# Kernel tuning notes

Measured on AMD Instinct MI355X. Metric: run time of the kernel, lower is better.

The kernel has to match this reference:

```python
import jax, jax.numpy as jnp
import numpy as np

B = 32768          # batch (replay-buffer minibatch)
OBS, ACT = 17, 6   # HalfCheetah-style dims
IN = OBS + ACT
H = 256            # hidden width hard-coded in the module
N = 10             # num_q_nets


def setup_inputs() -> dict:
    key = jax.random.key(0)
    ks = jax.random.split(key, 8)
    # PyTorch Linear default init: U(-1/sqrt(fan_in), 1/sqrt(fan_in)); scale randn similarly.
    s1, s2, s3 = 1.0 / np.sqrt(IN), 1.0 / np.sqrt(H), 1.0 / np.sqrt(H)
    return {
        "state": jax.random.normal(ks[0], (B, OBS), dtype=jnp.float32),
        "action": jax.random.uniform(ks[1], (B, ACT), dtype=jnp.float32, minval=-1.0, maxval=1.0),
        "W1": jax.random.normal(ks[2], (N, IN, H), dtype=jnp.float32) * s1,
        "b1": jax.random.normal(ks[3], (N, H), dtype=jnp.float32) * s1,
        "W2": jax.random.normal(ks[4], (N, H, H), dtype=jnp.float32) * s2,
        "b2": jax.random.normal(ks[5], (N, H), dtype=jnp.float32) * s2,
        "W3": jax.random.normal(ks[6], (N, H, 1), dtype=jnp.float32) * s3,
        "b3": jax.random.normal(ks[7], (N, 1), dtype=jnp.float32) * s3,
    }


def reference(state, action, W1, b1, W2, b2, W3, b3):
    # x: [B, OBS+ACT]
    x = jnp.concatenate([state, action], axis=1)
    # batched-over-ensemble GEMMs; n=ensemble member, b=batch
    h1 = jax.nn.relu(jnp.einsum("bi,nih->nbh", x, W1) + b1[:, None, :])   # [N,B,H]
    h2 = jax.nn.relu(jnp.einsum("nbh,nho->nbo", h1, W2) + b2[:, None, :])  # [N,B,H]
    out = jnp.einsum("nbh,nho->nbo", h2, W3) + b3[:, None, :]              # [N,B,1]
    return out
```

## Files before the change

### kernel.cpp

```cpp
#include <hip/hip_runtime.h>


typedef __attribute__((ext_vector_type(8))) short bf16x8;
typedef __attribute__((ext_vector_type(4))) float f32x4;

#define B_TOTAL 32768
#define NQ 10
#define HDIM 256
#define BT 128

__device__ __forceinline__ unsigned short f2bf(float f) {
  unsigned int u = __float_as_uint(f);
  u = u + 0x7FFFu + ((u >> 16) & 1u);
  return (unsigned short)(u >> 16);
}
__device__ __forceinline__ float bf2f(unsigned short h) {
  return __uint_as_float(((unsigned int)h) << 16);
}


__global__ void pack_x_kernel(const float* __restrict__ state,
                              const float* __restrict__ action,
                              unsigned short* __restrict__ xp) {
  int t = blockIdx.x * 256 + threadIdx.x;
  if (t >= B_TOTAL * 32) return;
  int b = t >> 5, k = t & 31;
  float v = 0.f;
  if (k < 17) v = state[b * 17 + k];
  else if (k < 23) v = action[b * 6 + (k - 17)];
  xp[t] = f2bf(v);
}

__global__ void pack_w1_kernel(const float* __restrict__ W1, unsigned short* __restrict__ w1p) {
  int t = blockIdx.x * 256 + threadIdx.x;
  if (t >= NQ * 16 * 64) return;
  int lane = t & 63;
  int ct = (t >> 6) & 15;
  int n = t >> 10;
  int c = ct * 16 + (lane & 15);
  int q = lane >> 4;
#pragma unroll
  for (int j = 0; j < 8; j++) {
    int k = q * 8 + j;
    float v = (k < 23) ? W1[(n * 23 + k) * 256 + c] : 0.f;
    w1p[(size_t)t * 8 + j] = f2bf(v);
  }
}

__global__ void pack_w2_kernel(const float* __restrict__ W2, unsigned short* __restrict__ w2p) {
  int t = blockIdx.x * 256 + threadIdx.x;
  if (t >= NQ * 8 * 16 * 64) return;
  int lane = t & 63;
  int ct = (t >> 6) & 15;
  int kt = (t >> 10) & 7;
  int n = t >> 13;
  int c = ct * 16 + (lane & 15);
  int q = lane >> 4;
#pragma unroll
  for (int j = 0; j < 8; j++) {
    int k = kt * 32 + q * 8 + j;
    w2p[(size_t)t * 8 + j] = f2bf(W2[((size_t)n * 256 + k) * 256 + c]);
  }
}

__global__ __launch_bounds__(256, 2) void fused_ensemble_kernel(
    const unsigned short* __restrict__ xp,
    const unsigned short* __restrict__ w1p,
    const float* __restrict__ b1,
    const unsigned short* __restrict__ w2p,
    const float* __restrict__ b2,
    const float* __restrict__ W3,
    const float* __restrict__ b3,
    float* __restrict__ out) {
  __shared__ __align__(16) unsigned short xs[BT * 40];
  __shared__ __align__(16) unsigned short h1s[BT * 264];
  __shared__ float w3s[HDIM];

  const int tid = threadIdx.x;
  const int lane = tid & 63;
  const int wave = tid >> 6;
  const int m = lane & 15;
  const int q = lane >> 4;

  const int n = blockIdx.x >> 8;
  const int tile = blockIdx.x & 255;
  const int row0 = tile * BT;

  {
    const uint4* src = (const uint4*)(xp + (size_t)row0 * 32);
#pragma unroll
    for (int i = 0; i < 2; i++) {
      int idx = tid + i * 256;
      int r = idx >> 2, c4 = idx & 3;
      uint4 v = src[idx];
      *(uint4*)&xs[r * 40 + c4 * 8] = v;
    }
  }
  if (tid < HDIM) w3s[tid] = W3[n * HDIM + tid];
  __syncthreads();

  f32x4 acc[8][4];
#pragma unroll
  for (int a = 0; a < 8; a++)
#pragma unroll
    for (int b = 0; b < 4; b++) acc[a][b] = (f32x4){0.f, 0.f, 0.f, 0.f};

  {
    bf16x8 bfrag[4];
#pragma unroll
    for (int cti = 0; cti < 4; cti++) {
      int ct = wave * 4 + cti;
      bfrag[cti] = *(const bf16x8*)(w1p + (((size_t)n * 16 + ct) * 64 + lane) * 8);
    }
#pragma unroll
    for (int mt = 0; mt < 8; mt++) {
      bf16x8 afrag = *(const bf16x8*)&xs[(mt * 16 + m) * 40 + q * 8];
#pragma unroll
      for (int cti = 0; cti < 4; cti++)
        acc[mt][cti] = __builtin_amdgcn_mfma_f32_16x16x32_bf16(afrag, bfrag[cti], acc[mt][cti], 0, 0, 0);
    }
  }

#pragma unroll
  for (int cti = 0; cti < 4; cti++) {
    int col = (wave * 4 + cti) * 16 + m;
    float bias = b1[n * HDIM + col];
#pragma unroll
    for (int mt = 0; mt < 8; mt++)
#pragma unroll
      for (int r = 0; r < 4; r++) {
        float v = acc[mt][cti][r] + bias;
        h1s[(mt * 16 + q * 4 + r) * 264 + col] = f2bf(v > 0.f ? v : 0.f);
      }
  }
  __syncthreads();

#pragma unroll
  for (int a = 0; a < 8; a++)
#pragma unroll
    for (int b = 0; b < 4; b++) acc[a][b] = (f32x4){0.f, 0.f, 0.f, 0.f};

  const unsigned short* w2n = w2p + (size_t)n * 8 * 16 * 512;
  bf16x8 bcur[4], bnxt[4];
#pragma unroll
  for (int cti = 0; cti < 4; cti++)
    bcur[cti] = *(const bf16x8*)(w2n + (((size_t)(wave * 4 + cti)) * 64 + lane) * 8);

  for (int kt = 0; kt < 8; kt++) {
    if (kt < 7) {
#pragma unroll
      for (int cti = 0; cti < 4; cti++)
        bnxt[cti] = *(const bf16x8*)(w2n + (((size_t)(kt + 1) * 16 + wave * 4 + cti) * 64 + lane) * 8);
    }
    bf16x8 afrag[8];
#pragma unroll
    for (int mt = 0; mt < 8; mt++)
      afrag[mt] = *(const bf16x8*)&h1s[(mt * 16 + m) * 264 + kt * 32 + q * 8];
#pragma unroll
    for (int mt = 0; mt < 8; mt++)
#pragma unroll
      for (int cti = 0; cti < 4; cti++)
        acc[mt][cti] = __builtin_amdgcn_mfma_f32_16x16x32_bf16(afrag[mt], bcur[cti], acc[mt][cti], 0, 0, 0);
#pragma unroll
    for (int cti = 0; cti < 4; cti++) bcur[cti] = bnxt[cti];
  }
  __syncthreads();

#pragma unroll
  for (int cti = 0; cti < 4; cti++) {
    int col = (wave * 4 + cti) * 16 + m;
    float bias = b2[n * HDIM + col];
#pragma unroll
    for (int mt = 0; mt < 8; mt++)
#pragma unroll
      for (int r = 0; r < 4; r++) {
        float v = acc[mt][cti][r] + bias;
        h1s[(mt * 16 + q * 4 + r) * 264 + col] = f2bf(v > 0.f ? v : 0.f);
      }
  }
  __syncthreads();

  {
    int row = tid >> 1;
    int half = tid & 1;
    const unsigned short* hrow = &h1s[row * 264 + half * 128];
    const float* wrow = &w3s[half * 128];
    float s = 0.f;
#pragma unroll
    for (int i = 0; i < 16; i++) {
      bf16x8 hv = *(const bf16x8*)(hrow + i * 8);
#pragma unroll
      for (int j = 0; j < 8; j++)
        s += bf2f((unsigned short)hv[j]) * wrow[i * 8 + j];
    }
    s += __shfl_xor(s, 1);
    if (half == 0) out[(size_t)n * B_TOTAL + row0 + row] = s + b3[n];
  }
}

extern "C" void kernel_launch(void* const* d_in, const int* in_sizes, int n_in,
                              void* d_out, int out_size, void* d_ws, size_t ws_size,
                              hipStream_t stream) {
  const float* state  = (const float*)d_in[0];
  const float* action = (const float*)d_in[1];
  const float* W1 = (const float*)d_in[2];
  const float* b1 = (const float*)d_in[3];
  const float* W2 = (const float*)d_in[4];
  const float* b2 = (const float*)d_in[5];
  const float* W3 = (const float*)d_in[6];
  const float* b3 = (const float*)d_in[7];
  float* out = (float*)d_out;

  unsigned short* xp  = (unsigned short*)d_ws;
  unsigned short* w1p = (unsigned short*)((char*)d_ws + 2097152);
  unsigned short* w2p = (unsigned short*)((char*)d_ws + 2097152 + 163840);

  pack_x_kernel<<<(B_TOTAL * 32) / 256, 256, 0, stream>>>(state, action, xp);
  pack_w1_kernel<<<40, 256, 0, stream>>>(W1, w1p);
  pack_w2_kernel<<<320, 256, 0, stream>>>(W2, w2p);
  fused_ensemble_kernel<<<NQ * (B_TOTAL / BT), 256, 0, stream>>>(
      xp, w1p, b1, w2p, b2, W3, b3, out);
}
```

Measured before the change: 141.1 us.

## Fuse input packing into main kernel, swap GEMM operand roles, MFMA final layer

Drops the separate x-packing kernel: each block now converts its own state/action rows to bf16 in shared memory, and the three weight-pack kernels are merged into one launch. The MFMA operands are swapped so weights become the A operand. This lets bias be preloaded into the accumulators and lets activations be written to shared memory as packed 4-element bf16 stores. The final 256-to-1 layer is computed with MFMA against a zero-padded W3 fragment instead of a scalar dot product. The cost is redundant x conversion across the 10 ensemble blocks that share a tile, uncoalesced stride-17 loads, and MFMA work wasted on the padding.

```diff
diff --git a/kernel.cpp b/kernel.cpp
--- a/kernel.cpp
+++ b/kernel.cpp
@@ -1,4 +1,5 @@
 #include <hip/hip_runtime.h>
+#include <hip/hip_bf16.h>
 
 
 typedef __attribute__((ext_vector_type(8))) short bf16x8;
@@ -8,73 +9,79 @@
 #define NQ 10
 #define HDIM 256
 #define BT 128
+#define XS_STRIDE 40
+#define H_STRIDE 264
+
+#define W1P_ELEMS (NQ * 16 * 64 * 8)
+#define W2P_ELEMS (NQ * 8 * 16 * 64 * 8)
+#define W3P_ELEMS (NQ * 8 * 64 * 8)
 
 __device__ __forceinline__ unsigned short f2bf(float f) {
   unsigned int u = __float_as_uint(f);
   u = u + 0x7FFFu + ((u >> 16) & 1u);
   return (unsigned short)(u >> 16);
 }
-__device__ __forceinline__ float bf2f(unsigned short h) {
-  return __uint_as_float(((unsigned int)h) << 16);
-}
-
-
-__global__ void pack_x_kernel(const float* __restrict__ state,
-                              const float* __restrict__ action,
-                              unsigned short* __restrict__ xp) {
+
+__device__ __forceinline__ unsigned int pk2bf(float a, float b) {
+  union { __hip_bfloat162 h; unsigned int u; } cv;
+  cv.h = __float22bfloat162_rn(make_float2(a, b));
+  return cv.u;
+}
+
+__global__ void pack_weights_kernel(const float* __restrict__ W1,
+                                    const float* __restrict__ W2,
+                                    const float* __restrict__ W3,
+                                    unsigned short* __restrict__ w1p,
+                                    unsigned short* __restrict__ w2p,
+                                    unsigned short* __restrict__ w3p) {
   int t = blockIdx.x * 256 + threadIdx.x;
-  if (t >= B_TOTAL * 32) return;
-  int b = t >> 5, k = t & 31;
-  float v = 0.f;
-  if (k < 17) v = state[b * 17 + k];
-  else if (k < 23) v = action[b * 6 + (k - 17)];
-  xp[t] = f2bf(v);
-}
-
-__global__ void pack_w1_kernel(const float* __restrict__ W1, unsigned short* __restrict__ w1p) {
-  int t = blockIdx.x * 256 + threadIdx.x;
-  if (t >= NQ * 16 * 64) return;
-  int lane = t & 63;
-  int ct = (t >> 6) & 15;
-  int n = t >> 10;
-  int c = ct * 16 + (lane & 15);
-  int q = lane >> 4;
-#pragma unroll
-  for (int j = 0; j < 8; j++) {
-    int k = q * 8 + j;
-    float v = (k < 23) ? W1[(n * 23 + k) * 256 + c] : 0.f;
-    w1p[(size_t)t * 8 + j] = f2bf(v);
-  }
-}
-
-__global__ void pack_w2_kernel(const float* __restrict__ W2, unsigned short* __restrict__ w2p) {
-  int t = blockIdx.x * 256 + threadIdx.x;
-  if (t >= NQ * 8 * 16 * 64) return;
-  int lane = t & 63;
-  int ct = (t >> 6) & 15;
-  int kt = (t >> 10) & 7;
-  int n = t >> 13;
-  int c = ct * 16 + (lane & 15);
-  int q = lane >> 4;
-#pragma unroll
-  for (int j = 0; j < 8; j++) {
-    int k = kt * 32 + q * 8 + j;
-    w2p[(size_t)t * 8 + j] = f2bf(W2[((size_t)n * 256 + k) * 256 + c]);
+  const int NW1 = NQ * 16 * 64;
+  const int NW2 = NQ * 8 * 16 * 64;
+  if (t < NW1) {
+    int lane = t & 63, mt = (t >> 6) & 15, n = t >> 10;
+    int m = lane & 15, q = lane >> 4;
+    int outc = mt * 16 + m;
+#pragma unroll
+    for (int j = 0; j < 8; j++) {
+      int k = q * 8 + j;
+      float v = (k < 23) ? W1[(n * 23 + k) * 256 + outc] : 0.f;
+      w1p[(size_t)t * 8 + j] = f2bf(v);
+    }
+  } else if (t < NW1 + NW2) {
+    int u = t - NW1;
+    int lane = u & 63, mt = (u >> 6) & 15, kt = (u >> 10) & 7, n = u >> 13;
+    int m = lane & 15, q = lane >> 4;
+    int outc = mt * 16 + m;
+#pragma unroll
+    for (int j = 0; j < 8; j++) {
+      int h = kt * 32 + q * 8 + j;
+      w2p[(size_t)u * 8 + j] = f2bf(W2[((size_t)(n * 256 + h)) * 256 + outc]);
+    }
+  } else {
+    int u = t - NW1 - NW2;
+    int lane = u & 63, kt = (u >> 6) & 7, n = u >> 9;
+    int m = lane & 15, q = lane >> 4;
+#pragma unroll
+    for (int j = 0; j < 8; j++) {
+      int h = kt * 32 + q * 8 + j;
+      float v = (m == 0) ? W3[n * 256 + h] : 0.f;
+      w3p[(size_t)u * 8 + j] = f2bf(v);
+    }
   }
 }
 
 __global__ __launch_bounds__(256, 2) void fused_ensemble_kernel(
-    const unsigned short* __restrict__ xp,
+    const float* __restrict__ state,
+    const float* __restrict__ action,
     const unsigned short* __restrict__ w1p,
     const float* __restrict__ b1,
     const unsigned short* __restrict__ w2p,
     const float* __restrict__ b2,
-    const float* __restrict__ W3,
+    const unsigned short* __restrict__ w3p,
     const float* __restrict__ b3,
     float* __restrict__ out) {
-  __shared__ __align__(16) unsigned short xs[BT * 40];
-  __shared__ __align__(16) unsigned short h1s[BT * 264];
-  __shared__ float w3s[HDIM];
+  __shared__ __align__(16) unsigned short xs[BT * XS_STRIDE];
+  __shared__ __align__(16) unsigned short hs[BT * H_STRIDE];
 
   const int tid = threadIdx.x;
   const int lane = tid & 63;
@@ -87,114 +94,125 @@
   const int row0 = tile * BT;
 
   {
-    const uint4* src = (const uint4*)(xp + (size_t)row0 * 32);
-#pragma unroll
-    for (int i = 0; i < 2; i++) {
-      int idx = tid + i * 256;
-      int r = idx >> 2, c4 = idx & 3;
-      uint4 v = src[idx];
-      *(uint4*)&xs[r * 40 + c4 * 8] = v;
-    }
-  }
-  if (tid < HDIM) w3s[tid] = W3[n * HDIM + tid];
-  __syncthreads();
-
-  f32x4 acc[8][4];
-#pragma unroll
-  for (int a = 0; a < 8; a++)
-#pragma unroll
-    for (int b = 0; b < 4; b++) acc[a][b] = (f32x4){0.f, 0.f, 0.f, 0.f};
-
-  {
-    bf16x8 bfrag[4];
-#pragma unroll
-    for (int cti = 0; cti < 4; cti++) {
-      int ct = wave * 4 + cti;
-      bfrag[cti] = *(const bf16x8*)(w1p + (((size_t)n * 16 + ct) * 64 + lane) * 8);
-    }
-#pragma unroll
-    for (int mt = 0; mt < 8; mt++) {
-      bf16x8 afrag = *(const bf16x8*)&xs[(mt * 16 + m) * 40 + q * 8];
-#pragma unroll
-      for (int cti = 0; cti < 4; cti++)
-        acc[mt][cti] = __builtin_amdgcn_mfma_f32_16x16x32_bf16(afrag, bfrag[cti], acc[mt][cti], 0, 0, 0);
-    }
-  }
-
-#pragma unroll
-  for (int cti = 0; cti < 4; cti++) {
-    int col = (wave * 4 + cti) * 16 + m;
-    float bias = b1[n * HDIM + col];
-#pragma unroll
-    for (int mt = 0; mt < 8; mt++)
-#pragma unroll
-      for (int r = 0; r < 4; r++) {
-        float v = acc[mt][cti][r] + bias;
-        h1s[(mt * 16 + q * 4 + r) * 264 + col] = f2bf(v > 0.f ? v : 0.f);
+    const float* sp = state + (size_t)row0 * 17;
+    for (int i = tid; i < BT * 17; i += 256) {
+      int b = i / 17, k = i - b * 17;
+      xs[b * XS_STRIDE + k] = f2bf(sp[i]);
+    }
+    const float* ap = action + (size_t)row0 * 6;
+    for (int i = tid; i < BT * 6; i += 256) {
+      int b = i / 6, k = i - b * 6;
+      xs[b * XS_STRIDE + 17 + k] = f2bf(ap[i]);
+    }
+    for (int i = tid; i < BT * 9; i += 256) {
+      int b = i / 9, k = i - b * 9;
+      xs[b * XS_STRIDE + 23 + k] = 0;
+    }
+  }
+  __syncthreads();
+
+  f32x4 acc[4][8];
+
+  {
+    bf16x8 afrag[4];
+#pragma unroll
+    for (int mt = 0; mt < 4; mt++)
+      afrag[mt] = *(const bf16x8*)(w1p + (((size_t)n * 16 + wave * 4 + mt) * 64 + lane) * 8);
+#pragma unroll
+    for (int mt = 0; mt < 4; mt++) {
+      float4 bv = *(const float4*)&b1[n * HDIM + (wave * 4 + mt) * 16 + q * 4];
+      f32x4 bi = (f32x4){bv.x, bv.y, bv.z, bv.w};
+#pragma unroll
+      for (int nt = 0; nt < 8; nt++) acc[mt][nt] = bi;
+    }
+#pragma unroll
+    for (int nt = 0; nt < 8; nt++) {
+      bf16x8 bfrag = *(const bf16x8*)&xs[(nt * 16 + m) * XS_STRIDE + q * 8];
+#pragma unroll
+      for (int mt = 0; mt < 4; mt++)
+        acc[mt][nt] = __builtin_amdgcn_mfma_f32_16x16x32_bf16(afrag[mt], bfrag, acc[mt][nt], 0, 0, 0);
+    }
+  }
+
+#pragma unroll
+  for (int mt = 0; mt < 4; mt++)
+#pragma unroll
+    for (int nt = 0; nt < 8; nt++) {
+      f32x4 a = acc[mt][nt];
+      uint2 w;
+      w.x = pk2bf(fmaxf(a[0], 0.f), fmaxf(a[1], 0.f));
+      w.y = pk2bf(fmaxf(a[2], 0.f), fmaxf(a[3], 0.f));
+      *(uint2*)&hs[(nt * 16 + m) * H_STRIDE + (wave * 4 + mt) * 16 + q * 4] = w;
+    }
+  __syncthreads();
+
+  {
+    const unsigned short* w2n = w2p + (size_t)n * (8 * 16 * 64 * 8);
+    bf16x8 acur[4], anxt[4];
+#pragma unroll
+    for (int mt = 0; mt < 4; mt++)
+      acur[mt] = *(const bf16x8*)(w2n + (((size_t)(wave * 4 + mt)) * 64 + lane) * 8);
+#pragma unroll
+    for (int mt = 0; mt < 4; mt++) {
+      float4 bv = *(const float4*)&b2[n * HDIM + (wave * 4 + mt) * 16 + q * 4];
+      f32x4 bi = (f32x4){bv.x, bv.y, bv.z, bv.w};
+#pragma unroll
+      for (int nt = 0; nt < 8; nt++) acc[mt][nt] = bi;
+    }
+#pragma unroll
+    for (int kt = 0; kt < 8; kt++) {
+      if (kt < 7) {
+#pragma unroll
+        for (int mt = 0; mt < 4; mt++)
+          anxt[mt] = *(const bf16x8*)(w2n + (((size_t)(kt + 1) * 16 + wave * 4 + mt) * 64 + lane) * 8);
       }
-  }
-  __syncthreads();
-
-#pragma unroll
-  for (int a = 0; a < 8; a++)
-#pragma unroll
-    for (int b = 0; b < 4; b++) acc[a][b] = (f32x4){0.f, 0.f, 0.f, 0.f};
-
-  const unsigned short* w2n = w2p + (size_t)n * 8 * 16 * 512;
-  bf16x8 bcur[4], bnxt[4];
-#pragma unroll
-  for (int cti = 0; cti < 4; cti++)
-    bcur[cti] = *(const bf16x8*)(w2n + (((size_t)(wave * 4 + cti)) * 64 + lane) * 8);
-
-  for (int kt = 0; kt < 8; kt++) {
-    if (kt < 7) {
-#pragma unroll
-      for (int cti = 0; cti < 4; cti++)
-        bnxt[cti] = *(const bf16x8*)(w2n + (((size_t)(kt + 1) * 16 + wave * 4 + cti) * 64 + lane) * 8);
-    }
-    bf16x8 afrag[8];
-#pragma unroll
-    for (int mt = 0; mt < 8; mt++)
-      afrag[mt] = *(const bf16x8*)&h1s[(mt * 16 + m) * 264 + kt * 32 + q * 8];
-#pragma unroll
-    for (int mt = 0; mt < 8; mt++)
-#pragma unroll
-      for (int cti = 0; cti < 4; cti++)
-        acc[mt][cti] = __builtin_amdgcn_mfma_f32_16x16x32_bf16(afrag[mt], bcur[cti], acc[mt][cti], 0, 0, 0);
-#pragma unroll
-    for (int cti = 0; cti < 4; cti++) bcur[cti] = bnxt[cti];
-  }
-  __syncthreads();
-
-#pragma unroll
-  for (int cti = 0; cti < 4; cti++) {
-    int col = (wave * 4 + cti) * 16 + m;
-    float bias = b2[n * HDIM + col];
-#pragma unroll
-    for (int mt = 0; mt < 8; mt++)
-#pragma unroll
-      for (int r = 0; r < 4; r++) {
-        float v = acc[mt][cti][r] + bias;
-        h1s[(mt * 16 + q * 4 + r) * 264 + col] = f2bf(v > 0.f ? v : 0.f);
+      bf16x8 bfrag[8];
+#pragma unroll
+      for (int nt = 0; nt < 8; nt++)
+        bfrag[nt] = *(const bf16x8*)&hs[(nt * 16 + m) * H_STRIDE + kt * 32 + q * 8];
+#pragma unroll
+      for (int nt = 0; nt < 8; nt++)
+#pragma unroll
+        for (int mt = 0; mt < 4; mt++)
+          acc[mt][nt] = __builtin_amdgcn_mfma_f32_16x16x32_bf16(acur[mt], bfrag[nt], acc[mt][nt], 0, 0, 0);
+#pragma unroll
+      for (int mt = 0; mt < 4; mt++) acur[mt] = anxt[mt];
+    }
+  }
+  __syncthreads();
+
+#pragma unroll
+  for (int mt = 0; mt < 4; mt++)
+#pragma unroll
+    for (int nt = 0; nt < 8; nt++) {
+      f32x4 a = acc[mt][nt];
+      uint2 w;
+      w.x = pk2bf(fmaxf(a[0], 0.f), fmaxf(a[1], 0.f));
+      w.y = pk2bf(fmaxf(a[2], 0.f), fmaxf(a[3], 0.f));
+      *(uint2*)&hs[(nt * 16 + m) * H_STRIDE + (wave * 4 + mt) * 16 + q * 4] = w;
+    }
+  __syncthreads();
+
+  {
+    const unsigned short* w3n = w3p + (size_t)n * (8 * 64 * 8);
+    f32x4 acc3[2];
+    acc3[0] = (f32x4){0.f, 0.f, 0.f, 0.f};
+    acc3[1] = (f32x4){0.f, 0.f, 0.f, 0.f};
+#pragma unroll
+    for (int kt = 0; kt < 8; kt++) {
+      bf16x8 af = *(const bf16x8*)(w3n + ((size_t)kt * 64 + lane) * 8);
+#pragma unroll
+      for (int i = 0; i < 2; i++) {
+        bf16x8 bf_ = *(const bf16x8*)&hs[((wave * 2 + i) * 16 + m) * H_STRIDE + kt * 32 + q * 8];
+        acc3[i] = __builtin_amdgcn_mfma_f32_16x16x32_bf16(af, bf_, acc3[i], 0, 0, 0);
       }
-  }
-  __syncthreads();
-
-  {
-    int row = tid >> 1;
-    int half = tid & 1;
-    const unsigned short* hrow = &h1s[row * 264 + half * 128];
-    const float* wrow = &w3s[half * 128];
-    float s = 0.f;
-#pragma unroll
-    for (int i = 0; i < 16; i++) {
-      bf16x8 hv = *(const bf16x8*)(hrow + i * 8);
-#pragma unroll
-      for (int j = 0; j < 8; j++)
-        s += bf2f((unsigned short)hv[j]) * wrow[i * 8 + j];
-    }
-    s += __shfl_xor(s, 1);
-    if (half == 0) out[(size_t)n * B_TOTAL + row0 + row] = s + b3[n];
+    }
+    if (lane < 16) {
+      float bias = b3[n];
+#pragma unroll
+      for (int i = 0; i < 2; i++)
+        out[(size_t)n * B_TOTAL + row0 + (wave * 2 + i) * 16 + m] = acc3[i][0] + bias;
+    }
   }
 }
 
@@ -211,13 +229,11 @@
   const float* b3 = (const float*)d_in[7];
   float* out = (float*)d_out;
 
-  unsigned short* xp  = (unsigned short*)d_ws;
-  unsigned short* w1p = (unsigned short*)((char*)d_ws + 2097152);
-  unsigned short* w2p = (unsigned short*)((char*)d_ws + 2097152 + 163840);
-
-  pack_x_kernel<<<(B_TOTAL * 32) / 256, 256, 0, stream>>>(state, action, xp);
-  pack_w1_kernel<<<40, 256, 0, stream>>>(W1, w1p);
-  pack_w2_kernel<<<320, 256, 0, stream>>>(W2, w2p);
+  unsigned short* w1p = (unsigned short*)d_ws;
+  unsigned short* w2p = (unsigned short*)((char*)d_ws + (size_t)W1P_ELEMS * 2);
+  unsigned short* w3p = (unsigned short*)((char*)d_ws + (size_t)(W1P_ELEMS + W2P_ELEMS) * 2);
+
+  pack_weights_kernel<<<380, 256, 0, stream>>>(W1, W2, W3, w1p, w2p, w3p);
   fused_ensemble_kernel<<<NQ * (B_TOTAL / BT), 256, 0, stream>>>(
-      xp, w1p, b1, w2p, b2, W3, b3, out);
-}
+      state, action, w1p, b1, w2p, b2, w3p, b3, out);
+}
```

After: 132.5 us. 1.07x faster.
